# Kernel optimization log

Measured on AMD Instinct MI355X. Metric: run time of the kernel, lower is better.

The kernel has to match this reference:

```python
import jax, jax.numpy as jnp
import numpy as np

GROUPS = 8
EPS = 1e-5


def group_norm(x, gamma, beta):
    # x: [B, C, H, W]; normalize per group over (C/g, H, W)
    B, C, H, W = x.shape
    xg = x.reshape(B, GROUPS, C // GROUPS, H, W)
    mean = xg.mean(axis=(2, 3, 4), keepdims=True)
    var = xg.var(axis=(2, 3, 4), keepdims=True)
    xg = (xg - mean) * jax.lax.rsqrt(var + EPS)
    x = xg.reshape(B, C, H, W)
    return x * gamma[None, :, None, None] + beta[None, :, None, None]


def setup_inputs() -> dict:
    key = jax.random.key(0)
    ks = jax.random.split(key, 6)
    B, C, H, W = 8, 512, 32, 32
    x = jax.random.normal(ks[0], (B, C, H, W), dtype=jnp.float32)
    gn_w = jnp.ones((C,), dtype=jnp.float32)
    gn_b = jnp.zeros((C,), dtype=jnp.float32)
    s = 1.0 / np.sqrt(C)
    qkv_w = jax.random.uniform(ks[1], (3 * C, C), minval=-s, maxval=s, dtype=jnp.float32)
    qkv_b = jax.random.uniform(ks[2], (3 * C,), minval=-s, maxval=s, dtype=jnp.float32)
    proj_w = jax.random.uniform(ks[3], (C, C), minval=-s, maxval=s, dtype=jnp.float32)
    proj_b = jax.random.uniform(ks[4], (C,), minval=-s, maxval=s, dtype=jnp.float32)
    return {"x": x, "gn_w": gn_w, "gn_b": gn_b, "qkv_w": qkv_w,
            "qkv_b": qkv_b, "proj_w": proj_w, "proj_b": proj_b}


def reference(x, gn_w, gn_b, qkv_w, qkv_b, proj_w, proj_b):
    B, C, H, W = x.shape
    xn = group_norm(x, gn_w, gn_b)              # [B,C,H,W] (also the residual)
    xf = xn.reshape(B, C, H * W).transpose(0, 2, 1)  # [B,N,C]
    qkv = jnp.einsum('bnc,dc->bnd', xf, qkv_w) + qkv_b  # [B,N,3C]
    q, k, v = jnp.split(qkv, 3, axis=-1)
    k = jax.nn.softmax(k, axis=-1)              # over channels
    q = jax.nn.softmax(q, axis=-2)              # over tokens
    context = jnp.einsum('bnc,bnd->bcd', k, v)  # [B,C,C]
    out = jnp.einsum('bnc,bcd->bnd', q, context)  # [B,N,C]
    out = jnp.einsum('bnc,dc->bnd', out, proj_w) + proj_b
    out = out.transpose(0, 2, 1).reshape(B, C, H, W)
    return out + xn
```

## Files before the change

### kernel.cpp

```cpp
#include <hip/hip_runtime.h>
#include <hip/hip_bf16.h>
#include <stdint.h>

typedef unsigned short u16;
typedef __attribute__((ext_vector_type(8))) short s16x8;
typedef __attribute__((ext_vector_type(4))) float f32x4;
typedef __attribute__((ext_vector_type(4))) unsigned short u16x4;

static constexpr int B_ = 8, C_ = 512, N_ = 1024, G_ = 8;
static constexpr float EPS = 1e-5f;

static constexpr size_t OFF_XNT  = 0;
static constexpr size_t OFF_Q    = OFF_XNT  + (size_t)B_*N_*C_*2;
static constexpr size_t OFF_K    = OFF_Q    + (size_t)B_*N_*C_*2;
static constexpr size_t OFF_V    = OFF_K    + (size_t)B_*N_*C_*2;
static constexpr size_t OFF_KT   = OFF_V    + (size_t)B_*N_*C_*2;
static constexpr size_t OFF_VT   = OFF_KT   + (size_t)B_*N_*C_*2;
static constexpr size_t OFF_QS   = OFF_VT   + (size_t)B_*N_*C_*2;
static constexpr size_t OFF_CTXT = OFF_QS   + (size_t)B_*N_*C_*2;
static constexpr size_t OFF_ATT  = OFF_CTXT + (size_t)B_*C_*C_*2;
static constexpr size_t OFF_WQ   = OFF_ATT  + (size_t)B_*N_*C_*2;
static constexpr size_t OFF_WP   = OFF_WQ   + (size_t)3*C_*C_*2;
static constexpr size_t OFF_GNP  = OFF_WP   + (size_t)C_*C_*2;

__device__ __forceinline__ float b2f(u16 u) {
  union { float f; uint32_t i; } x; x.i = ((uint32_t)u) << 16; return x.f;
}
__device__ __forceinline__ u16 f2b(float f) {
  union { float f; uint32_t i; } x; x.f = f;
  return (u16)((x.i + 0x7fffu + ((x.i >> 16) & 1u)) >> 16);
}
#define AS1 __attribute__((address_space(1)))
#define AS3 __attribute__((address_space(3)))
__device__ __forceinline__ void gl2lds16(const void* g, void* l) {
  __builtin_amdgcn_global_load_lds((const AS1 void*)g, (AS3 void*)l, 16, 0, 0);
}

__global__ __launch_bounds__(256) void gn_partial(const float* __restrict__ x,
                                                  float* __restrict__ gnp) {
  int bg = blockIdx.x;
  int chunk = blockIdx.y;
  const float4* p = reinterpret_cast<const float4*>(x + (size_t)bg * 65536 + (size_t)chunk * 8192);
  int tid = threadIdx.x;
  float s = 0.f, sq = 0.f;
#pragma unroll
  for (int i = 0; i < 8; ++i) {
    float4 v = p[i * 256 + tid];
    s  += v.x + v.y + v.z + v.w;
    sq += v.x*v.x + v.y*v.y + v.z*v.z + v.w*v.w;
  }
  for (int off = 32; off; off >>= 1) { s += __shfl_xor(s, off); sq += __shfl_xor(sq, off); }
  __shared__ float red[8];
  int wid = tid >> 6, lane = tid & 63;
  if (lane == 0) { red[wid*2] = s; red[wid*2+1] = sq; }
  __syncthreads();
  if (tid == 0) {
    gnp[(bg*8 + chunk)*2 + 0] = red[0]+red[2]+red[4]+red[6];
    gnp[(bg*8 + chunk)*2 + 1] = red[1]+red[3]+red[5]+red[7];
  }
}

__global__ __launch_bounds__(256) void gn_apply(const float* __restrict__ x,
                                                const float* __restrict__ gw,
                                                const float* __restrict__ gb,
                                                const float* __restrict__ gnp,
                                                u16* __restrict__ xnT) {
  __shared__ float T[64][65];
  int b = blockIdx.x, c0 = blockIdx.y * 64, n0 = blockIdx.z * 64;
  int bg = b * G_ + blockIdx.y;
  float S = 0.f, SQ = 0.f;
#pragma unroll
  for (int i = 0; i < 8; ++i) { S += gnp[(bg*8+i)*2]; SQ += gnp[(bg*8+i)*2+1]; }
  float mean = S * (1.f/65536.f);
  float var  = SQ * (1.f/65536.f) - mean*mean;
  float rstd = rsqrtf(var + EPS);
  int tn = threadIdx.x & 63, tc = threadIdx.x >> 6;
#pragma unroll 4
  for (int it = 0; it < 16; ++it) {
    int cl = it*4 + tc;
    int c = c0 + cl;
    float v = x[((size_t)b*C_ + c)*N_ + n0 + tn];
    T[tn][cl] = (v - mean) * rstd * gw[c] + gb[c];
  }
  __syncthreads();
#pragma unroll
  for (int p = 0; p < 2; ++p) {
    int nl = p*32 + (threadIdx.x >> 3);
    int cs = (threadIdx.x & 7) * 8;
    s16x8 o;
#pragma unroll
    for (int j = 0; j < 8; ++j) o[j] = (short)f2b(T[nl][cs + j]);
    *reinterpret_cast<s16x8*>(&xnT[((size_t)(b*N_ + n0 + nl))*C_ + c0 + cs]) = o;
  }
}

__global__ __launch_bounds__(256) void cvt_w2(const float* __restrict__ w1,
                                              const float* __restrict__ w2,
                                              u16* __restrict__ o1,
                                              u16* __restrict__ o2) {
  int i = blockIdx.x * 256 + threadIdx.x;
  const int n1 = 1536*512/4;
  if (i < n1) {
    float4 v = reinterpret_cast<const float4*>(w1)[i];
    u16x4 r = { f2b(v.x), f2b(v.y), f2b(v.z), f2b(v.w) };
    reinterpret_cast<u16x4*>(o1)[i] = r;
  } else {
    int j = i - n1;
    float4 v = reinterpret_cast<const float4*>(w2)[j];
    u16x4 r = { f2b(v.x), f2b(v.y), f2b(v.z), f2b(v.w) };
    reinterpret_cast<u16x4*>(o2)[j] = r;
  }
}

template<int EPI>
__global__ __launch_bounds__(256) void gemm(const u16* __restrict__ A,
                                            const u16* __restrict__ Bm,
                                            int M, int N, int K, int lda, int ldb,
                                            long strideA, long strideB, long strideC,
                                            const float* __restrict__ bias,
                                            void* __restrict__ O0,
                                            const void* __restrict__ R) {
  constexpr int BM = 128, BN = 128, BK = 64;
  __shared__ u16 As[2][BM*BK];
  __shared__ u16 Bs[2][BN*BK];
  int tid = threadIdx.x, wid = tid >> 6, lane = tid & 63;
  int m0 = blockIdx.x * BM, n0 = blockIdx.y * BN;
  const u16* Ab = A + (size_t)strideA * blockIdx.z;
  const u16* Bp = Bm + (size_t)strideB * blockIdx.z;

  f32x4 acc[4][4] = {};
  int wm = (wid >> 1) * 64, wn = (wid & 1) * 64;
  int sr = lane >> 3;
  int sg = (lane & 7) ^ sr;

  auto stage = [&](int buf, int k0) {
#pragma unroll
    for (int t = 0; t < 4; ++t) {
      int chunk = wid*4 + t;
      gl2lds16(Ab + (size_t)(m0 + chunk*8 + sr)*lda + k0 + sg*8,
               (void*)(&As[buf][chunk*512]));
      gl2lds16(Bp + (size_t)(n0 + chunk*8 + sr)*ldb + k0 + sg*8,
               (void*)(&Bs[buf][chunk*512]));
    }
  };

  int KT = K / BK;
  stage(0, 0);
  __syncthreads();
  int cur = 0;
  for (int kt = 0; kt < KT; ++kt) {
    if (kt + 1 < KT) stage(cur ^ 1, (kt + 1) * BK);
#pragma unroll
    for (int ks = 0; ks < BK; ks += 32) {
      int s = (ks >> 3) + (lane >> 4);
      s16x8 af[4], bfr[4];
#pragma unroll
      for (int mi = 0; mi < 4; ++mi) {
        int ar = wm + mi*16 + (lane & 15);
        af[mi] = *reinterpret_cast<const s16x8*>(&As[cur][ar*64 + ((s ^ (ar & 7)) << 3)]);
      }
#pragma unroll
      for (int ni = 0; ni < 4; ++ni) {
        int br = wn + ni*16 + (lane & 15);
        bfr[ni] = *reinterpret_cast<const s16x8*>(&Bs[cur][br*64 + ((s ^ (br & 7)) << 3)]);
      }
#pragma unroll
      for (int mi = 0; mi < 4; ++mi)
#pragma unroll
        for (int ni = 0; ni < 4; ++ni)
          acc[mi][ni] = __builtin_amdgcn_mfma_f32_16x16x32_bf16(af[mi], bfr[ni], acc[mi][ni], 0, 0, 0);
    }
    __syncthreads();
    cur ^= 1;
  }

#pragma unroll
  for (int mi = 0; mi < 4; ++mi) {
#pragma unroll
    for (int ni = 0; ni < 4; ++ni) {
      int col = n0 + wn + ni*16 + (lane & 15);
      if constexpr (EPI == 2) {
        int rowb = m0 + wm + mi*16 + (lane >> 4)*4;
        int b = rowb >> 10, n = rowb & 1023;
        const u16* xr = (const u16*)R + ((size_t)(b*N_ + n))*C_ + col;
        size_t idx = (size_t)b*524288 + (size_t)col*1024 + n;
        float bi = bias[col];
        float4 o;
        o.x = acc[mi][ni][0] + bi + b2f(xr[0]);
        o.y = acc[mi][ni][1] + bi + b2f(xr[512]);
        o.z = acc[mi][ni][2] + bi + b2f(xr[1024]);
        o.w = acc[mi][ni][3] + bi + b2f(xr[1536]);
        *reinterpret_cast<float4*>((float*)O0 + idx) = o;
      } else {
#pragma unroll
        for (int r = 0; r < 4; ++r) {
          int row = m0 + wm + mi*16 + (lane >> 4)*4 + r;
          ((u16*)O0)[(size_t)strideC*blockIdx.z + (size_t)row*N + col] = f2b(acc[mi][ni][r]);
        }
      }
    }
  }
}

__global__ __launch_bounds__(256) void gemm_qkv(const u16* __restrict__ A,
                                                const u16* __restrict__ Bm,
                                                const float* __restrict__ bias,
                                                u16* __restrict__ Oq,
                                                u16* __restrict__ Ok,
                                                u16* __restrict__ Ov) {
  constexpr int BM = 128, BN = 128, BK = 64;
  const int lda = 512, ldb = 512;
  __shared__ u16 As[2][BM*BK];
  __shared__ u16 Bs[2][BN*BK];
  int tid = threadIdx.x, wid = tid >> 6, lane = tid & 63;
  int m0 = blockIdx.x * BM, n0 = blockIdx.y * BN;

  f32x4 acc[4][4] = {};
  int wm = (wid >> 1) * 64, wn = (wid & 1) * 64;
  int sr = lane >> 3;
  int sg = (lane & 7) ^ sr;

  auto stage = [&](int buf, int k0) {
#pragma unroll
    for (int t = 0; t < 4; ++t) {
      int chunk = wid*4 + t;
      gl2lds16(A + (size_t)(m0 + chunk*8 + sr)*lda + k0 + sg*8,
               (void*)(&As[buf][chunk*512]));
      gl2lds16(Bm + (size_t)(n0 + chunk*8 + sr)*ldb + k0 + sg*8,
               (void*)(&Bs[buf][chunk*512]));
    }
  };

  stage(0, 0);
  __syncthreads();
  int cur = 0;
  for (int kt = 0; kt < 8; ++kt) {
    if (kt + 1 < 8) stage(cur ^ 1, (kt + 1) * BK);
#pragma unroll
    for (int ks = 0; ks < BK; ks += 32) {
      int s = (ks >> 3) + (lane >> 4);
      s16x8 af[4], bfr[4];
#pragma unroll
      for (int mi = 0; mi < 4; ++mi) {
        int ar = wm + mi*16 + (lane & 15);
        af[mi] = *reinterpret_cast<const s16x8*>(&As[cur][ar*64 + ((s ^ (ar & 7)) << 3)]);
      }
#pragma unroll
      for (int ni = 0; ni < 4; ++ni) {
        int br = wn + ni*16 + (lane & 15);
        bfr[ni] = *reinterpret_cast<const s16x8*>(&Bs[cur][br*64 + ((s ^ (br & 7)) << 3)]);
      }
#pragma unroll
      for (int mi = 0; mi < 4; ++mi)
#pragma unroll
        for (int ni = 0; ni < 4; ++ni)
          acc[mi][ni] = __builtin_amdgcn_mfma_f32_16x16x32_bf16(af[mi], bfr[ni], acc[mi][ni], 0, 0, 0);
    }
    __syncthreads();
    cur ^= 1;
  }

  u16* Odst; int cbase;
  if (n0 < 512)       { Odst = Oq; cbase = n0; }
  else if (n0 < 1024) { Odst = Ok; cbase = n0 - 512; }
  else                { Odst = Ov; cbase = n0 - 1024; }
#pragma unroll
  for (int mi = 0; mi < 4; ++mi) {
#pragma unroll
    for (int ni = 0; ni < 4; ++ni) {
      int col = n0 + wn + ni*16 + (lane & 15);
      int c   = cbase + wn + ni*16 + (lane & 15);
      float bi = bias[col];
#pragma unroll
      for (int r = 0; r < 4; ++r) {
        int row = m0 + wm + mi*16 + (lane >> 4)*4 + r;
        Odst[(size_t)row*512 + c] = f2b(acc[mi][ni][r] + bi);
      }
    }
  }
}

__global__ __launch_bounds__(256) void kv_transform(const u16* __restrict__ kin,
                                                    const u16* __restrict__ vin,
                                                    u16* __restrict__ kT,
                                                    u16* __restrict__ vT) {
  __shared__ u16 T[32][516];
  int b = blockIdx.x, n0 = blockIdx.y * 32;
  int wid = threadIdx.x >> 6, lane = threadIdx.x & 63;

#pragma unroll
  for (int i = 0; i < 8; ++i) {
    int r = wid * 8 + i;
    const u16* p = kin + ((size_t)(b*N_ + n0 + r))*C_;
    s16x8 raw = reinterpret_cast<const s16x8*>(p)[lane];
    float v[8]; float m = -3e38f;
#pragma unroll
    for (int j = 0; j < 8; ++j) { v[j] = b2f((u16)raw[j]); m = fmaxf(m, v[j]); }
    for (int off = 32; off; off >>= 1) m = fmaxf(m, __shfl_xor(m, off));
    float s = 0.f;
#pragma unroll
    for (int j = 0; j < 8; ++j) { v[j] = __expf(v[j] - m); s += v[j]; }
    for (int off = 32; off; off >>= 1) s += __shfl_xor(s, off);
    float inv = 1.f / s;
    union { s16x8 v8; unsigned long long d[2]; } o;
#pragma unroll
    for (int j = 0; j < 8; ++j) o.v8[j] = (short)f2b(v[j] * inv);
    unsigned long long* dst = reinterpret_cast<unsigned long long*>(&T[r][lane*8]);
    dst[0] = o.d[0]; dst[1] = o.d[1];
  }
  __syncthreads();
#pragma unroll
  for (int h = 0; h < 2; ++h) {
    int c = h*256 + threadIdx.x;
    u16* dst = kT + ((size_t)(b*C_ + c))*N_ + n0;
#pragma unroll
    for (int q4 = 0; q4 < 4; ++q4) {
      s16x8 o;
#pragma unroll
      for (int j = 0; j < 8; ++j) o[j] = (short)T[q4*8 + j][c];
      reinterpret_cast<s16x8*>(dst)[q4] = o;
    }
  }
  __syncthreads();

#pragma unroll
  for (int i = 0; i < 8; ++i) {
    int r = wid * 8 + i;
    const u16* p = vin + ((size_t)(b*N_ + n0 + r))*C_;
    union { s16x8 v8; unsigned long long d[2]; } o;
    o.v8 = reinterpret_cast<const s16x8*>(p)[lane];
    unsigned long long* dst = reinterpret_cast<unsigned long long*>(&T[r][lane*8]);
    dst[0] = o.d[0]; dst[1] = o.d[1];
  }
  __syncthreads();
#pragma unroll
  for (int h = 0; h < 2; ++h) {
    int c = h*256 + threadIdx.x;
    u16* dst = vT + ((size_t)(b*C_ + c))*N_ + n0;
#pragma unroll
    for (int q4 = 0; q4 < 4; ++q4) {
      s16x8 o;
#pragma unroll
      for (int j = 0; j < 8; ++j) o[j] = (short)T[q4*8 + j][c];
      reinterpret_cast<s16x8*>(dst)[q4] = o;
    }
  }
}

__global__ __launch_bounds__(256) void q_softmax(const u16* __restrict__ q,
                                                 u16* __restrict__ qs) {
  int b = blockIdx.x, c0 = blockIdx.y * 32;
  int t = threadIdx.x;
  int cg = t & 3;
  int rw = t >> 2;
  const u16* base = q + (size_t)b*N_*C_ + c0 + cg*8;
  float m[8], s[8];
#pragma unroll
  for (int j = 0; j < 8; ++j) { m[j] = -3e38f; s[j] = 0.f; }
  for (int it = 0; it < 16; ++it) {
    int n = it*64 + rw;
    s16x8 raw = *reinterpret_cast<const s16x8*>(base + (size_t)n*C_);
#pragma unroll
    for (int j = 0; j < 8; ++j) {
      float v = b2f((u16)raw[j]);
      float nm = fmaxf(m[j], v);
      s[j] = s[j]*__expf(m[j] - nm) + __expf(v - nm);
      m[j] = nm;
    }
  }
  __shared__ float Mr[32][65], Sr[32][65];
#pragma unroll
  for (int j = 0; j < 8; ++j) { Mr[cg*8 + j][rw] = m[j]; Sr[cg*8 + j][rw] = s[j]; }
  __syncthreads();
  __shared__ float MS[32][2];
  if (t < 32) {
    float M = -3e38f;
    for (int i = 0; i < 64; ++i) M = fmaxf(M, Mr[t][i]);
    float S = 0.f;
    for (int i = 0; i < 64; ++i) S += Sr[t][i]*__expf(Mr[t][i] - M);
    MS[t][0] = M; MS[t][1] = 1.f / S;
  }
  __syncthreads();
  float Mv[8], Iv[8];
#pragma unroll
  for (int j = 0; j < 8; ++j) { Mv[j] = MS[cg*8 + j][0]; Iv[j] = MS[cg*8 + j][1]; }
  u16* ob = qs + (size_t)b*N_*C_ + c0 + cg*8;
  for (int it = 0; it < 16; ++it) {
    int n = it*64 + rw;
    s16x8 raw = *reinterpret_cast<const s16x8*>(base + (size_t)n*C_);
    s16x8 o;
#pragma unroll
    for (int j = 0; j < 8; ++j)
      o[j] = (short)f2b(__expf(b2f((u16)raw[j]) - Mv[j]) * Iv[j]);
    *reinterpret_cast<s16x8*>(ob + (size_t)n*C_) = o;
  }
}

extern "C" void kernel_launch(void* const* d_in, const int* in_sizes, int n_in,
                              void* d_out, int out_size, void* d_ws, size_t ws_size,
                              hipStream_t stream) {
  (void)in_sizes; (void)n_in; (void)out_size; (void)ws_size;
  const float* x      = (const float*)d_in[0];
  const float* gn_w   = (const float*)d_in[1];
  const float* gn_b   = (const float*)d_in[2];
  const float* qkv_w  = (const float*)d_in[3];
  const float* qkv_b  = (const float*)d_in[4];
  const float* proj_w = (const float*)d_in[5];
  const float* proj_b = (const float*)d_in[6];

  char* ws = (char*)d_ws;
  u16*   xnT  = (u16*)  (ws + OFF_XNT);
  u16*   qb   = (u16*)  (ws + OFF_Q);
  u16*   kb   = (u16*)  (ws + OFF_K);
  u16*   vb   = (u16*)  (ws + OFF_V);
  u16*   kT   = (u16*)  (ws + OFF_KT);
  u16*   vT   = (u16*)  (ws + OFF_VT);
  u16*   qsb  = (u16*)  (ws + OFF_QS);
  u16*   ctxT = (u16*)  (ws + OFF_CTXT);
  u16*   att  = (u16*)  (ws + OFF_ATT);
  u16*   wq   = (u16*)  (ws + OFF_WQ);
  u16*   wp   = (u16*)  (ws + OFF_WP);
  float* gnp  = (float*)(ws + OFF_GNP);

  gn_partial<<<dim3(64, 8), 256, 0, stream>>>(x, gnp);
  gn_apply<<<dim3(8, 8, 16), 256, 0, stream>>>(x, gn_w, gn_b, gnp, xnT);

  cvt_w2<<<dim3(1024), 256, 0, stream>>>(qkv_w, proj_w, wq, wp);

  gemm_qkv<<<dim3(64, 12), 256, 0, stream>>>(xnT, wq, qkv_b, qb, kb, vb);

  kv_transform<<<dim3(8, 32), 256, 0, stream>>>(kb, vb, kT, vT);
  q_softmax<<<dim3(8, 16), 256, 0, stream>>>(qb, qsb);

  gemm<1><<<dim3(4, 4, 8), 256, 0, stream>>>(vT, kT, 512, 512, 1024, 1024, 1024,
                                             524288, 524288, 262144, nullptr, ctxT, nullptr);
  gemm<1><<<dim3(8, 4, 8), 256, 0, stream>>>(qsb, ctxT, 1024, 512, 512, 512, 512,
                                             524288, 262144, 524288, nullptr, att, nullptr);
  gemm<2><<<dim3(64, 4), 256, 0, stream>>>(att, wp, 8192, 512, 512, 512, 512,
                                           0, 0, 0, proj_b, (float*)d_out, xnT);
}
```

Baseline: 185.5 us.

## Fold projection weight into context matrix and use smaller GEMM tiles

```diff
diff --git a/kernel.cpp b/kernel.cpp
--- a/kernel.cpp
+++ b/kernel.cpp
@@ -17,9 +17,9 @@
 static constexpr size_t OFF_KT   = OFF_V    + (size_t)B_*N_*C_*2;
 static constexpr size_t OFF_VT   = OFF_KT   + (size_t)B_*N_*C_*2;
 static constexpr size_t OFF_QS   = OFF_VT   + (size_t)B_*N_*C_*2;
-static constexpr size_t OFF_CTXT = OFF_QS   + (size_t)B_*N_*C_*2;
-static constexpr size_t OFF_ATT  = OFF_CTXT + (size_t)B_*C_*C_*2;
-static constexpr size_t OFF_WQ   = OFF_ATT  + (size_t)B_*N_*C_*2;
+static constexpr size_t OFF_CTX  = OFF_QS   + (size_t)B_*N_*C_*2;
+static constexpr size_t OFF_MT   = OFF_CTX  + (size_t)B_*C_*C_*2;
+static constexpr size_t OFF_WQ   = OFF_MT   + (size_t)B_*C_*C_*2;
 static constexpr size_t OFF_WP   = OFF_WQ   + (size_t)3*C_*C_*2;
 static constexpr size_t OFF_GNP  = OFF_WP   + (size_t)C_*C_*2;
 
@@ -112,7 +112,7 @@
   }
 }
 
-template<int EPI>
+template<int BM, int BN, int EPI>
 __global__ __launch_bounds__(256) void gemm(const u16* __restrict__ A,
                                             const u16* __restrict__ Bm,
                                             int M, int N, int K, int lda, int ldb,
@@ -120,7 +120,8 @@
                                             const float* __restrict__ bias,
                                             void* __restrict__ O0,
                                             const void* __restrict__ R) {
-  constexpr int BM = 128, BN = 128, BK = 64;
+  constexpr int BK = 64;
+  constexpr int MI = BM / 32, NI = BN / 32;
   __shared__ u16 As[2][BM*BK];
   __shared__ u16 Bs[2][BN*BK];
   int tid = threadIdx.x, wid = tid >> 6, lane = tid & 63;
@@ -128,17 +129,21 @@
   const u16* Ab = A + (size_t)strideA * blockIdx.z;
   const u16* Bp = Bm + (size_t)strideB * blockIdx.z;
 
-  f32x4 acc[4][4] = {};
-  int wm = (wid >> 1) * 64, wn = (wid & 1) * 64;
+  f32x4 acc[MI][NI] = {};
+  int wm = (wid >> 1) * (BM/2), wn = (wid & 1) * (BN/2);
   int sr = lane >> 3;
   int sg = (lane & 7) ^ sr;
 
   auto stage = [&](int buf, int k0) {
 #pragma unroll
-    for (int t = 0; t < 4; ++t) {
-      int chunk = wid*4 + t;
+    for (int t = 0; t < BM/32; ++t) {
+      int chunk = wid*(BM/32) + t;
       gl2lds16(Ab + (size_t)(m0 + chunk*8 + sr)*lda + k0 + sg*8,
                (void*)(&As[buf][chunk*512]));
+    }
+#pragma unroll
+    for (int t = 0; t < BN/32; ++t) {
+      int chunk = wid*(BN/32) + t;
       gl2lds16(Bp + (size_t)(n0 + chunk*8 + sr)*ldb + k0 + sg*8,
                (void*)(&Bs[buf][chunk*512]));
     }
@@ -153,21 +158,21 @@
 #pragma unroll
     for (int ks = 0; ks < BK; ks += 32) {
       int s = (ks >> 3) + (lane >> 4);
-      s16x8 af[4], bfr[4];
-#pragma unroll
-      for (int mi = 0; mi < 4; ++mi) {
+      s16x8 af[MI], bfr[NI];
+#pragma unroll
+      for (int mi = 0; mi < MI; ++mi) {
         int ar = wm + mi*16 + (lane & 15);
         af[mi] = *reinterpret_cast<const s16x8*>(&As[cur][ar*64 + ((s ^ (ar & 7)) << 3)]);
       }
 #pragma unroll
-      for (int ni = 0; ni < 4; ++ni) {
+      for (int ni = 0; ni < NI; ++ni) {
         int br = wn + ni*16 + (lane & 15);
         bfr[ni] = *reinterpret_cast<const s16x8*>(&Bs[cur][br*64 + ((s ^ (br & 7)) << 3)]);
       }
 #pragma unroll
-      for (int mi = 0; mi < 4; ++mi)
-#pragma unroll
-        for (int ni = 0; ni < 4; ++ni)
+      for (int mi = 0; mi < MI; ++mi)
+#pragma unroll
+        for (int ni = 0; ni < NI; ++ni)
           acc[mi][ni] = __builtin_amdgcn_mfma_f32_16x16x32_bf16(af[mi], bfr[ni], acc[mi][ni], 0, 0, 0);
     }
     __syncthreads();
@@ -175,13 +180,13 @@
   }
 
 #pragma unroll
-  for (int mi = 0; mi < 4; ++mi) {
-#pragma unroll
-    for (int ni = 0; ni < 4; ++ni) {
+  for (int mi = 0; mi < MI; ++mi) {
+#pragma unroll
+    for (int ni = 0; ni < NI; ++ni) {
       int col = n0 + wn + ni*16 + (lane & 15);
       if constexpr (EPI == 2) {
-        int rowb = m0 + wm + mi*16 + (lane >> 4)*4;
-        int b = rowb >> 10, n = rowb & 1023;
+        int n = m0 + wm + mi*16 + (lane >> 4)*4;
+        int b = blockIdx.z;
         const u16* xr = (const u16*)R + ((size_t)(b*N_ + n))*C_ + col;
         size_t idx = (size_t)b*524288 + (size_t)col*1024 + n;
         float bi = bias[col];
@@ -416,8 +421,8 @@
   u16*   kT   = (u16*)  (ws + OFF_KT);
   u16*   vT   = (u16*)  (ws + OFF_VT);
   u16*   qsb  = (u16*)  (ws + OFF_QS);
-  u16*   ctxT = (u16*)  (ws + OFF_CTXT);
-  u16*   att  = (u16*)  (ws + OFF_ATT);
+  u16*   ctx  = (u16*)  (ws + OFF_CTX);
+  u16*   mt   = (u16*)  (ws + OFF_MT);
   u16*   wq   = (u16*)  (ws + OFF_WQ);
   u16*   wp   = (u16*)  (ws + OFF_WP);
   float* gnp  = (float*)(ws + OFF_GNP);
@@ -432,10 +437,10 @@
   kv_transform<<<dim3(8, 32), 256, 0, stream>>>(kb, vb, kT, vT);
   q_softmax<<<dim3(8, 16), 256, 0, stream>>>(qb, qsb);
 
-  gemm<1><<<dim3(4, 4, 8), 256, 0, stream>>>(vT, kT, 512, 512, 1024, 1024, 1024,
-                                             524288, 524288, 262144, nullptr, ctxT, nullptr);
-  gemm<1><<<dim3(8, 4, 8), 256, 0, stream>>>(qsb, ctxT, 1024, 512, 512, 512, 512,
-                                             524288, 262144, 524288, nullptr, att, nullptr);
-  gemm<2><<<dim3(64, 4), 256, 0, stream>>>(att, wp, 8192, 512, 512, 512, 512,
-                                           0, 0, 0, proj_b, (float*)d_out, xnT);
-}
+  gemm<64,64,1><<<dim3(8, 8, 8), 256, 0, stream>>>(kT, vT, 512, 512, 1024, 1024, 1024,
+                                                   524288, 524288, 262144, nullptr, ctx, nullptr);
+  gemm<64,64,1><<<dim3(8, 8, 8), 256, 0, stream>>>(wp, ctx, 512, 512, 512, 512, 512,
+                                                   0, 262144, 262144, nullptr, mt, nullptr);
+  gemm<64,64,2><<<dim3(16, 8, 8), 256, 0, stream>>>(qsb, mt, 1024, 512, 512, 512, 512,
+                                                    524288, 262144, 0, proj_b, (float*)d_out, xnT);
+}
```

Result: faster. 172.2 us (-7.2%).
